# Kernel tuning notes

Measured on AMD Instinct MI355X. Metric: run time of the kernel, lower is better.

Reference implementation:

```python
import jax, jax.numpy as jnp
import numpy as np

N_NODES = 100000
N_EDGES = 1600000
D_IN = 128
D_HID = 128


def setup_inputs() -> dict:
    key = jax.random.key(0)
    ks = jax.random.split(key, 8)
    x = jax.random.normal(ks[0], (N_NODES, D_IN), dtype=jnp.float32)
    edge_index = jax.random.randint(ks[1], (2, N_EDGES), 0, N_NODES, dtype=jnp.int64)
    s = 1.0 / np.sqrt(D_IN)
    W_root1 = jax.random.normal(ks[2], (D_IN, D_HID), dtype=jnp.float32) * s
    W_rel1 = jax.random.normal(ks[3], (D_IN, D_HID), dtype=jnp.float32) * s
    b1 = jnp.zeros((D_HID,), dtype=jnp.float32)
    sh = 1.0 / np.sqrt(D_HID)
    W_root2 = jax.random.normal(ks[4], (D_HID, D_HID), dtype=jnp.float32) * sh
    W_rel2 = jax.random.normal(ks[5], (D_HID, D_HID), dtype=jnp.float32) * sh
    b2 = jnp.zeros((D_HID,), dtype=jnp.float32)
    return {"x": x, "edge_index": edge_index, "W_root1": W_root1, "W_rel1": W_rel1,
            "b1": b1, "W_root2": W_root2, "W_rel2": W_rel2, "b2": b2}


def graph_conv(x, src, dst, W_root, W_rel, b):
    # PyG GraphConv: out_i = x_i @ W_root + (sum_{j in N(i)} x_j) @ W_rel + b
    agg = jax.ops.segment_sum(x[src], dst, num_segments=N_NODES)  # [N, d]
    return x @ W_root + agg @ W_rel + b


def reference(x, edge_index, W_root1, W_rel1, b1, W_root2, W_rel2, b2):
    src, dst = edge_index[0], edge_index[1]
    h = jax.nn.relu(graph_conv(x, src, dst, W_root1, W_rel1, b1))
    # dropout is identity in eval mode (reference baseline)
    h = jax.nn.relu(graph_conv(h, src, dst, W_root2, W_rel2, b2))
    return h
```

## Files before the change

kernel.cpp:

```cpp
#include <hip/hip_runtime.h>

#define D 128
#define KTOT 256
#define GM 128
#define LPAD 8
#define LSTR (KTOT + LPAD)

#define EB1   8192
#define BKT_W 64
#define WIN   1024
#define EMAX  8192
#define HB1MAX 2048

typedef __attribute__((ext_vector_type(8))) short bf16x8;
typedef __attribute__((ext_vector_type(4))) float f32x4;

__device__ __forceinline__ unsigned short f2b(float f) {
    unsigned int u = __float_as_uint(f);
    u += 0x7fffu + ((u >> 16) & 1u);
    return (unsigned short)(u >> 16);
}
__device__ __forceinline__ float blo(unsigned int u) { return __uint_as_float(u << 16); }
__device__ __forceinline__ float bhi(unsigned int u) { return __uint_as_float(u & 0xffff0000u); }

__global__ __launch_bounds__(256) void pack2_kernel(
    const void* __restrict__ ei, unsigned int* __restrict__ pk,
    unsigned short* __restrict__ bkt, int n_edges)
{
    const unsigned int* eiu = (const unsigned int*)ei;
    const int l = threadIdx.x & 63;
    unsigned int w0 = eiu[2 * l + 1];
    unsigned int w1 = eiu[2 * (l + 64) + 1];
    const int is64 = __all((w0 | w1) == 0u);

    int e = blockIdx.x * 256 + threadIdx.x;
    if (e >= n_edges) return;
    int s, d;
    if (is64) {
        const long long* p = (const long long*)ei;
        s = (int)p[e]; d = (int)p[n_edges + e];
    } else {
        const int* p = (const int*)ei;
        s = p[e]; d = p[n_edges + e];
    }
    pk[e]  = ((unsigned int)s << 6) | (unsigned int)(d & (BKT_W - 1));
    bkt[e] = (unsigned short)(d >> 6);
}

__global__ __launch_bounds__(256) void s1_count_kernel(
    const unsigned short* __restrict__ bkt, int n_edges, int nb1,
    int* __restrict__ C)
{
    __shared__ int h[HB1MAX];
    for (int i = threadIdx.x; i < nb1; i += 256) h[i] = 0;
    __syncthreads();
    const int e0 = blockIdx.x * EB1;
    const int e1 = min(e0 + EB1, n_edges);
    for (int e = e0 + threadIdx.x; e < e1; e += 256)
        atomicAdd(&h[bkt[e]], 1);
    __syncthreads();
    int* out = C + (long long)blockIdx.x * nb1;
    for (int i = threadIdx.x; i < nb1; i += 256) out[i] = h[i];
}

__global__ __launch_bounds__(1024) void scanA_kernel(
    const int* __restrict__ C, int* __restrict__ Cs,
    int* __restrict__ blockSums, int L, int nb1, int nblk1)
{
    __shared__ int sm[1024];
    const int tid = threadIdx.x;
    const int i = blockIdx.x * 1024 + tid;
    int v = 0;
    if (i < L) {
        int b = i / nblk1, k = i - b * nblk1;
        v = C[(long long)k * nb1 + b];
    }
    int val = v;
    sm[tid] = val;
    __syncthreads();
    for (int off = 1; off < 1024; off <<= 1) {
        int t = (tid >= off) ? sm[tid - off] : 0;
        __syncthreads();
        val += t;
        sm[tid] = val;
        __syncthreads();
    }
    if (i < L) Cs[i] = val - v;
    if (tid == 1023) blockSums[blockIdx.x] = val;
}

__global__ __launch_bounds__(1024) void scan2_kernel(int* __restrict__ bs, int nb)
{
    __shared__ int sm[1024];
    int t = threadIdx.x;
    int v = (t < nb) ? bs[t] : 0;
    int val = v;
    sm[t] = val;
    __syncthreads();
    for (int off = 1; off < 1024; off <<= 1) {
        int u = (t >= off) ? sm[t - off] : 0;
        __syncthreads();
        val += u;
        sm[t] = val;
        __syncthreads();
    }
    if (t < nb) bs[t] = val - v;
}

__global__ __launch_bounds__(1024) void scan3_kernel(
    int* __restrict__ arr, const int* __restrict__ blockSums, int n)
{
    const int i = blockIdx.x * 1024 + threadIdx.x;
    if (i >= n) return;
    arr[i] += blockSums[blockIdx.x];
}

__global__ __launch_bounds__(256) void s1_scatter_kernel(
    const unsigned short* __restrict__ bkt, const unsigned int* __restrict__ pk,
    const int* __restrict__ Cs, unsigned int* __restrict__ sorted,
    int n_edges, int nb1, int nblk1, int lo)
{
    __shared__ int cur[WIN];
    const int hi = min(lo + WIN, nb1);
    for (int t = threadIdx.x; t < hi - lo; t += 256)
        cur[t] = Cs[(long long)(lo + t) * nblk1 + blockIdx.x];
    __syncthreads();
    const int e0 = blockIdx.x * EB1;
    const int e1 = min(e0 + EB1, n_edges);
    for (int e = e0 + threadIdx.x; e < e1; e += 256) {
        int b = bkt[e];
        if (b >= lo && b < hi) {
            int pos = atomicAdd(&cur[b - lo], 1);
            sorted[pos] = pk[e];
        }
    }
}

__global__ __launch_bounds__(256) void bucket_sort_kernel(
    unsigned int* __restrict__ sorted, const int* __restrict__ Cs,
    int n_edges, int n_nodes, int nb1, int nblk1, int* __restrict__ row_end)
{
    __shared__ unsigned int lpk[EMAX];
    __shared__ int h64[BKT_W], excl[BKT_W + 1], cur[BKT_W];
    const int b = blockIdx.x;
    const int t = threadIdx.x;
    const int base = Cs[(long long)b * nblk1];
    const int nextb = (b + 1 < nb1) ? Cs[(long long)(b + 1) * nblk1] : n_edges;
    const int cnt = min(nextb - base, EMAX);

    if (t < BKT_W) h64[t] = 0;
    for (int i = t; i < cnt; i += 256) lpk[i] = sorted[base + i];
    __syncthreads();
    for (int i = t; i < cnt; i += 256) atomicAdd(&h64[lpk[i] & (BKT_W - 1)], 1);
    __syncthreads();
    if (t == 0) {
        int run = 0;
        #pragma unroll
        for (int i = 0; i < BKT_W; ++i) { excl[i] = run; run += h64[i]; }
        excl[BKT_W] = run;
    }
    __syncthreads();
    const int node0 = b * BKT_W;
    const int bins = min(BKT_W, n_nodes - node0);
    if (t < bins) row_end[node0 + t] = base + excl[t + 1];
    if (t < BKT_W) cur[t] = excl[t];
    __syncthreads();
    for (int i = t; i < cnt; i += 256) {
        unsigned int p = lpk[i];
        int pos = atomicAdd(&cur[p & (BKT_W - 1)], 1);
        sorted[base + pos] = p >> 6;
    }
}

__global__ __launch_bounds__(256) void prep_kernel(
    const float* __restrict__ x, unsigned short* __restrict__ Xb,
    long long nelem, int nbcvt,
    const float* __restrict__ Wr1, const float* __restrict__ Wl1,
    unsigned short* __restrict__ Wt1,
    const float* __restrict__ Wr2, const float* __restrict__ Wl2,
    unsigned short* __restrict__ Wt2)
{
    const int b = blockIdx.x;
    if (b < nbcvt) {
        long long i = ((long long)b * 256 + threadIdx.x) * 8;
        if (i >= nelem) return;
        float4 a = *(const float4*)(x + i);
        float4 c = *(const float4*)(x + i + 4);
        bf16x8 v;
        v[0] = (short)f2b(a.x); v[1] = (short)f2b(a.y);
        v[2] = (short)f2b(a.z); v[3] = (short)f2b(a.w);
        v[4] = (short)f2b(c.x); v[5] = (short)f2b(c.y);
        v[6] = (short)f2b(c.z); v[7] = (short)f2b(c.w);
        *(bf16x8*)(Xb + i) = v;
    } else {
        const int cb = b - nbcvt;
        const float* Wr = (cb < 128) ? Wr1 : Wr2;
        const float* Wl = (cb < 128) ? Wl1 : Wl2;
        unsigned short* Wt = (cb < 128) ? Wt1 : Wt2;
        const int c = cb & 127;
        const int k = threadIdx.x;
        float v = (k < 128) ? Wr[k * D + c] : Wl[(k - 128) * D + c];
        Wt[c * KTOT + k] = f2b(v);
    }
}

#define ACC8(u) { a0 += blo(u.x); a1 += bhi(u.x); a2 += blo(u.y); a3 += bhi(u.y); \
                  a4 += blo(u.z); a5 += bhi(u.z); a6 += blo(u.w); a7 += bhi(u.w); }

__global__ __launch_bounds__(256) void agg_kernel(
    const unsigned short* __restrict__ src, const int* __restrict__ sorted_src,
    const int* __restrict__ row_end, unsigned short* __restrict__ dst, int n)
{
    const int node = blockIdx.x * 4 + (threadIdx.x >> 6);
    if (node >= n) return;
    const int lane = threadIdx.x & 63;
    const int j = lane >> 4;
    const int c = (lane & 15) * 8;
    const int beg = node ? row_end[node - 1] : 0;
    const int end = row_end[node];

    float a0 = 0.f, a1 = 0.f, a2 = 0.f, a3 = 0.f,
          a4 = 0.f, a5 = 0.f, a6 = 0.f, a7 = 0.f;

    int i = beg + j;
    for (; i + 12 < end; i += 16) {
        int s0 = sorted_src[i];
        int s1 = sorted_src[i + 4];
        int s2 = sorted_src[i + 8];
        int s3 = sorted_src[i + 12];
        uint4 u0 = *(const uint4*)(src + (long long)s0 * D + c);
        uint4 u1 = *(const uint4*)(src + (long long)s1 * D + c);
        uint4 u2 = *(const uint4*)(src + (long long)s2 * D + c);
        uint4 u3 = *(const uint4*)(src + (long long)s3 * D + c);
        ACC8(u0); ACC8(u1); ACC8(u2); ACC8(u3);
    }
    for (; i < end; i += 4) {
        int s0 = sorted_src[i];
        uint4 u0 = *(const uint4*)(src + (long long)s0 * D + c);
        ACC8(u0);
    }

    a0 += __shfl_xor(a0, 16); a1 += __shfl_xor(a1, 16);
    a2 += __shfl_xor(a2, 16); a3 += __shfl_xor(a3, 16);
    a4 += __shfl_xor(a4, 16); a5 += __shfl_xor(a5, 16);
    a6 += __shfl_xor(a6, 16); a7 += __shfl_xor(a7, 16);
    a0 += __shfl_xor(a0, 32); a1 += __shfl_xor(a1, 32);
    a2 += __shfl_xor(a2, 32); a3 += __shfl_xor(a3, 32);
    a4 += __shfl_xor(a4, 32); a5 += __shfl_xor(a5, 32);
    a6 += __shfl_xor(a6, 32); a7 += __shfl_xor(a7, 32);

    if (j == 0) {
        uint4 p;
        p.x = (unsigned int)f2b(a0) | ((unsigned int)f2b(a1) << 16);
        p.y = (unsigned int)f2b(a2) | ((unsigned int)f2b(a3) << 16);
        p.z = (unsigned int)f2b(a4) | ((unsigned int)f2b(a5) << 16);
        p.w = (unsigned int)f2b(a6) | ((unsigned int)f2b(a7) << 16);
        *(uint4*)(dst + (long long)node * D + c) = p;
    }
}

template <int OUT_BF16>
__global__ __launch_bounds__(512) void gemm_kernel(
    const unsigned short* __restrict__ Xop, const unsigned short* __restrict__ Aop,
    const unsigned short* __restrict__ Wt, const float* __restrict__ bias,
    void* outp, int n)
{
    __shared__ short sW[D][LSTR];
    const int tid = threadIdx.x;
    const int r0 = blockIdx.x * GM;

    for (int i = 0; i < 8; ++i) {
        int idx = tid + i * 512;
        int r = idx >> 5, c8 = idx & 31;
        bf16x8 w = *(const bf16x8*)(Wt + r * KTOT + c8 * 8);
        *(bf16x8*)&sW[r][c8 * 8] = w;
    }
    __syncthreads();

    const int w    = tid >> 6;
    const int lane = tid & 63;
    const int lr   = lane & 15;
    const int lk   = (lane >> 4) * 8;
    const int row  = r0 + w * 16 + lr;
    const bool rok = (row < n);

    f32x4 acc[8];
    #pragma unroll
    for (int ct = 0; ct < 8; ++ct) acc[ct] = (f32x4){0.f, 0.f, 0.f, 0.f};

    #pragma unroll
    for (int ks = 0; ks < 8; ++ks) {
        bf16x8 a = {};
        if (rok) {
            const unsigned short* base = (ks < 4) ? Xop : Aop;
            a = *(const bf16x8*)(base + (long long)row * D + (ks & 3) * 32 + lk);
        }
        #pragma unroll
        for (int ct = 0; ct < 8; ++ct) {
            bf16x8 bf = *(const bf16x8*)&sW[ct * 16 + lr][ks * 32 + lk];
            acc[ct] = __builtin_amdgcn_mfma_f32_16x16x32_bf16(a, bf, acc[ct], 0, 0, 0);
        }
    }

    const int rbase = r0 + w * 16 + (lane >> 4) * 4;
    #pragma unroll
    for (int ct = 0; ct < 8; ++ct) {
        const int col = ct * 16 + lr;
        const float bv = bias[col];
        #pragma unroll
        for (int j = 0; j < 4; ++j) {
            int orow = rbase + j;
            if (orow < n) {
                float val = fmaxf(acc[ct][j] + bv, 0.f);
                if (OUT_BF16) {
                    ((unsigned short*)outp)[(long long)orow * D + col] = f2b(val);
                } else {
                    ((float*)outp)[(long long)orow * D + col] = val;
                }
            }
        }
    }
}

static inline size_t align_up(size_t v, size_t a) { return (v + a - 1) & ~(a - 1); }

extern "C" void kernel_launch(void* const* d_in, const int* in_sizes, int n_in,
                              void* d_out, int out_size, void* d_ws, size_t ws_size,
                              hipStream_t stream) {
    const float* x   = (const float*)d_in[0];
    const void*  ei  = d_in[1];
    const float* Wr1 = (const float*)d_in[2];
    const float* Wl1 = (const float*)d_in[3];
    const float* b1  = (const float*)d_in[4];
    const float* Wr2 = (const float*)d_in[5];
    const float* Wl2 = (const float*)d_in[6];
    const float* b2  = (const float*)d_in[7];
    float* out = (float*)d_out;

    const int n_nodes = in_sizes[0] / D;
    const int n_edges = in_sizes[1] / 2;

    const int nb1   = (n_nodes + BKT_W - 1) / BKT_W;
    const int nblk1 = (n_edges + EB1 - 1) / EB1;
    const int L     = nb1 * nblk1;
    const int npass = (nb1 + WIN - 1) / WIN;
    const int nbL   = (L + 1023) / 1024;

    char* ws = (char*)d_ws;
    size_t off_rs   = 0;
    size_t off_bs   = align_up(off_rs + 4 * (size_t)(n_nodes + 1), 256);
    size_t off_ssrc = align_up(off_bs + 4 * 1024, 256);
    size_t off_wt1  = align_up(off_ssrc + 4 * (size_t)n_edges, 256);
    size_t off_wt2  = align_up(off_wt1 + 2 * (size_t)D * KTOT, 256);
    size_t off_xb   = align_up(off_wt2 + 2 * (size_t)D * KTOT, 256);
    size_t off_ab   = align_up(off_xb + 2 * (size_t)n_nodes * D, 256);

    int* row_end         = (int*)(ws + off_rs);
    int* blockSums       = (int*)(ws + off_bs);
    unsigned int* sorted = (unsigned int*)(ws + off_ssrc);
    unsigned short* Wt1  = (unsigned short*)(ws + off_wt1);
    unsigned short* Wt2  = (unsigned short*)(ws + off_wt2);
    unsigned short* Xb   = (unsigned short*)(ws + off_xb);
    unsigned short* Ab   = (unsigned short*)(ws + off_ab);
    unsigned int*   pk  = (unsigned int*)(ws + off_xb);
    unsigned short* bkt = (unsigned short*)(pk + n_edges);
    int* C  = (int*)(ws + off_ab);
    int* Cs = C + L;

    const int edge_blocks = (n_edges + 255) / 256;
    const int gemm_blocks = (n_nodes + GM - 1) / GM;
    const int agg_blocks  = (n_nodes + 3) / 4;
    const long long nfeat = (long long)n_nodes * D;
    const int nbcvt = (int)((nfeat / 8 + 255) / 256);

    pack2_kernel<<<edge_blocks, 256, 0, stream>>>(ei, pk, bkt, n_edges);
    s1_count_kernel<<<nblk1, 256, 0, stream>>>(bkt, n_edges, nb1, C);
    scanA_kernel<<<nbL, 1024, 0, stream>>>(C, Cs, blockSums, L, nb1, nblk1);
    scan2_kernel<<<1, 1024, 0, stream>>>(blockSums, nbL);
    scan3_kernel<<<nbL, 1024, 0, stream>>>(Cs, blockSums, L);
    for (int p = 0; p < npass; ++p) {
        s1_scatter_kernel<<<nblk1, 256, 0, stream>>>(
            bkt, pk, Cs, sorted, n_edges, nb1, nblk1, p * WIN);
    }

    prep_kernel<<<nbcvt + 256, 256, 0, stream>>>(
        x, Xb, nfeat, nbcvt, Wr1, Wl1, Wt1, Wr2, Wl2, Wt2);

    bucket_sort_kernel<<<nb1, 256, 0, stream>>>(
        sorted, Cs, n_edges, n_nodes, nb1, nblk1, row_end);

    agg_kernel<<<agg_blocks, 256, 0, stream>>>(Xb, (const int*)sorted, row_end, Ab, n_nodes);
    gemm_kernel<1><<<gemm_blocks, 512, 0, stream>>>(Xb, Ab, Wt1, b1, Ab, n_nodes);

    agg_kernel<<<agg_blocks, 256, 0, stream>>>(Ab, (const int*)sorted, row_end, Xb, n_nodes);
    gemm_kernel<0><<<gemm_blocks, 512, 0, stream>>>(Ab, Xb, Wt2, b2, out, n_nodes);
}
```

Baseline: 260.5 us.

## Store bf16 features in 16-column slices and aggregate one slice per block

Node features are stored in eight column slices of 16 bf16 values each (slice-major) instead of row-major. The aggregation kernel gets eight times as many blocks, one slice each, with 32 edges gathered in parallel per wave at 32 bytes per edge. Prep and GEMM indexing are changed to match the sliced layout. The aim is better gather parallelism and cache locality per slice. In exchange, neighbour indices are re-read once per slice, each gather is a small 32-byte fetch, and consecutive blocks touch different slices, which may weaken locality.

```diff
diff --git a/kernel.cpp b/kernel.cpp
--- a/kernel.cpp
+++ b/kernel.cpp
@@ -22,6 +22,10 @@
 }
 __device__ __forceinline__ float blo(unsigned int u) { return __uint_as_float(u << 16); }
 __device__ __forceinline__ float bhi(unsigned int u) { return __uint_as_float(u & 0xffff0000u); }
+
+__device__ __forceinline__ size_t sidx(int node, int c, size_t nS) {
+    return (size_t)(c >> 4) * nS + (size_t)node * 16 + (c & 15);
+}
 
 __global__ __launch_bounds__(256) void pack2_kernel(
     const void* __restrict__ ei, unsigned int* __restrict__ pk,
@@ -174,7 +178,7 @@
 
 __global__ __launch_bounds__(256) void prep_kernel(
     const float* __restrict__ x, unsigned short* __restrict__ Xb,
-    long long nelem, int nbcvt,
+    long long nelem, int nbcvt, size_t nS,
     const float* __restrict__ Wr1, const float* __restrict__ Wl1,
     unsigned short* __restrict__ Wt1,
     const float* __restrict__ Wr2, const float* __restrict__ Wl2,
@@ -185,13 +189,15 @@
         long long i = ((long long)b * 256 + threadIdx.x) * 8;
         if (i >= nelem) return;
         float4 a = *(const float4*)(x + i);
-        float4 c = *(const float4*)(x + i + 4);
+        float4 c2 = *(const float4*)(x + i + 4);
         bf16x8 v;
-        v[0] = (short)f2b(a.x); v[1] = (short)f2b(a.y);
-        v[2] = (short)f2b(a.z); v[3] = (short)f2b(a.w);
-        v[4] = (short)f2b(c.x); v[5] = (short)f2b(c.y);
-        v[6] = (short)f2b(c.z); v[7] = (short)f2b(c.w);
-        *(bf16x8*)(Xb + i) = v;
+        v[0] = (short)f2b(a.x);  v[1] = (short)f2b(a.y);
+        v[2] = (short)f2b(a.z);  v[3] = (short)f2b(a.w);
+        v[4] = (short)f2b(c2.x); v[5] = (short)f2b(c2.y);
+        v[6] = (short)f2b(c2.z); v[7] = (short)f2b(c2.w);
+        const int node = (int)(i >> 7);
+        const int c = (int)(i & 127);
+        *(bf16x8*)(Xb + sidx(node, c, nS)) = v;
     } else {
         const int cb = b - nbcvt;
         const float* Wr = (cb < 128) ? Wr1 : Wr2;
@@ -209,53 +215,43 @@
 
 __global__ __launch_bounds__(256) void agg_kernel(
     const unsigned short* __restrict__ src, const int* __restrict__ sorted_src,
-    const int* __restrict__ row_end, unsigned short* __restrict__ dst, int n)
-{
-    const int node = blockIdx.x * 4 + (threadIdx.x >> 6);
+    const int* __restrict__ row_end, unsigned short* __restrict__ dst,
+    int n, size_t nS)
+{
+    const int slice = blockIdx.x & 7;
+    const int node = (blockIdx.x >> 3) * 4 + (threadIdx.x >> 6);
     if (node >= n) return;
     const int lane = threadIdx.x & 63;
-    const int j = lane >> 4;
-    const int c = (lane & 15) * 8;
+    const int j    = lane >> 1;
+    const int half = lane & 1;
     const int beg = node ? row_end[node - 1] : 0;
     const int end = row_end[node];
+    const unsigned short* base = src + (size_t)slice * nS + half * 8;
 
     float a0 = 0.f, a1 = 0.f, a2 = 0.f, a3 = 0.f,
           a4 = 0.f, a5 = 0.f, a6 = 0.f, a7 = 0.f;
 
-    int i = beg + j;
-    for (; i + 12 < end; i += 16) {
-        int s0 = sorted_src[i];
-        int s1 = sorted_src[i + 4];
-        int s2 = sorted_src[i + 8];
-        int s3 = sorted_src[i + 12];
-        uint4 u0 = *(const uint4*)(src + (long long)s0 * D + c);
-        uint4 u1 = *(const uint4*)(src + (long long)s1 * D + c);
-        uint4 u2 = *(const uint4*)(src + (long long)s2 * D + c);
-        uint4 u3 = *(const uint4*)(src + (long long)s3 * D + c);
-        ACC8(u0); ACC8(u1); ACC8(u2); ACC8(u3);
-    }
-    for (; i < end; i += 4) {
-        int s0 = sorted_src[i];
-        uint4 u0 = *(const uint4*)(src + (long long)s0 * D + c);
-        ACC8(u0);
-    }
-
-    a0 += __shfl_xor(a0, 16); a1 += __shfl_xor(a1, 16);
-    a2 += __shfl_xor(a2, 16); a3 += __shfl_xor(a3, 16);
-    a4 += __shfl_xor(a4, 16); a5 += __shfl_xor(a5, 16);
-    a6 += __shfl_xor(a6, 16); a7 += __shfl_xor(a7, 16);
-    a0 += __shfl_xor(a0, 32); a1 += __shfl_xor(a1, 32);
-    a2 += __shfl_xor(a2, 32); a3 += __shfl_xor(a3, 32);
-    a4 += __shfl_xor(a4, 32); a5 += __shfl_xor(a5, 32);
-    a6 += __shfl_xor(a6, 32); a7 += __shfl_xor(a7, 32);
-
-    if (j == 0) {
+    for (int i = beg + j; i < end; i += 32) {
+        int s = sorted_src[i];
+        uint4 u = *(const uint4*)(base + (size_t)s * 16);
+        ACC8(u);
+    }
+
+    #pragma unroll
+    for (int m = 2; m <= 32; m <<= 1) {
+        a0 += __shfl_xor(a0, m); a1 += __shfl_xor(a1, m);
+        a2 += __shfl_xor(a2, m); a3 += __shfl_xor(a3, m);
+        a4 += __shfl_xor(a4, m); a5 += __shfl_xor(a5, m);
+        a6 += __shfl_xor(a6, m); a7 += __shfl_xor(a7, m);
+    }
+
+    if (lane < 2) {
         uint4 p;
         p.x = (unsigned int)f2b(a0) | ((unsigned int)f2b(a1) << 16);
         p.y = (unsigned int)f2b(a2) | ((unsigned int)f2b(a3) << 16);
         p.z = (unsigned int)f2b(a4) | ((unsigned int)f2b(a5) << 16);
         p.w = (unsigned int)f2b(a6) | ((unsigned int)f2b(a7) << 16);
-        *(uint4*)(dst + (long long)node * D + c) = p;
+        *(uint4*)(dst + (size_t)slice * nS + (size_t)node * 16 + half * 8) = p;
     }
 }
 
@@ -263,7 +259,7 @@
 __global__ __launch_bounds__(512) void gemm_kernel(
     const unsigned short* __restrict__ Xop, const unsigned short* __restrict__ Aop,
     const unsigned short* __restrict__ Wt, const float* __restrict__ bias,
-    void* outp, int n)
+    void* outp, int n, size_t nS)
 {
     __shared__ short sW[D][LSTR];
     const int tid = threadIdx.x;
@@ -292,8 +288,9 @@
     for (int ks = 0; ks < 8; ++ks) {
         bf16x8 a = {};
         if (rok) {
-            const unsigned short* base = (ks < 4) ? Xop : Aop;
-            a = *(const bf16x8*)(base + (long long)row * D + (ks & 3) * 32 + lk);
+            const unsigned short* bsrc = (ks < 4) ? Xop : Aop;
+            const int c0 = (ks & 3) * 32 + lk;
+            a = *(const bf16x8*)(bsrc + sidx(row, c0, nS));
         }
         #pragma unroll
         for (int ct = 0; ct < 8; ++ct) {
@@ -313,7 +310,7 @@
             if (orow < n) {
                 float val = fmaxf(acc[ct][j] + bv, 0.f);
                 if (OUT_BF16) {
-                    ((unsigned short*)outp)[(long long)orow * D + col] = f2b(val);
+                    ((unsigned short*)outp)[sidx(orow, col, nS)] = f2b(val);
                 } else {
                     ((float*)outp)[(long long)orow * D + col] = val;
                 }
@@ -339,6 +336,7 @@
 
     const int n_nodes = in_sizes[0] / D;
     const int n_edges = in_sizes[1] / 2;
+    const size_t nS   = (size_t)n_nodes * 16;
 
     const int nb1   = (n_nodes + BKT_W - 1) / BKT_W;
     const int nblk1 = (n_edges + EB1 - 1) / EB1;
@@ -369,7 +367,7 @@
 
     const int edge_blocks = (n_edges + 255) / 256;
     const int gemm_blocks = (n_nodes + GM - 1) / GM;
-    const int agg_blocks  = (n_nodes + 3) / 4;
+    const int agg_blocks  = ((n_nodes + 3) / 4) * 8;
     const long long nfeat = (long long)n_nodes * D;
     const int nbcvt = (int)((nfeat / 8 + 255) / 256);
 
@@ -384,14 +382,16 @@
     }
 
     prep_kernel<<<nbcvt + 256, 256, 0, stream>>>(
-        x, Xb, nfeat, nbcvt, Wr1, Wl1, Wt1, Wr2, Wl2, Wt2);
+        x, Xb, nfeat, nbcvt, nS, Wr1, Wl1, Wt1, Wr2, Wl2, Wt2);
 
     bucket_sort_kernel<<<nb1, 256, 0, stream>>>(
         sorted, Cs, n_edges, n_nodes, nb1, nblk1, row_end);
 
-    agg_kernel<<<agg_blocks, 256, 0, stream>>>(Xb, (const int*)sorted, row_end, Ab, n_nodes);
-    gemm_kernel<1><<<gemm_blocks, 512, 0, stream>>>(Xb, Ab, Wt1, b1, Ab, n_nodes);
-
-    agg_kernel<<<agg_blocks, 256, 0, stream>>>(Ab, (const int*)sorted, row_end, Xb, n_nodes);
-    gemm_kernel<0><<<gemm_blocks, 512, 0, stream>>>(Ab, Xb, Wt2, b2, out, n_nodes);
-}
+    agg_kernel<<<agg_blocks, 256, 0, stream>>>(
+        Xb, (const int*)sorted, row_end, Ab, n_nodes, nS);
+    gemm_kernel<1><<<gemm_blocks, 512, 0, stream>>>(Xb, Ab, Wt1, b1, Ab, n_nodes, nS);
+
+    agg_kernel<<<agg_blocks, 256, 0, stream>>>(
+        Ab, (const int*)sorted, row_end, Xb, n_nodes, nS);
+    gemm_kernel<0><<<gemm_blocks, 512, 0, stream>>>(Ab, Xb, Wt2, b2, out, n_nodes, nS);
+}
```

New measurement: 783.7 us. 3.01x slower.
